# Performance work log

Hardware: AMD Instinct MI355X
Metric: run time of the kernel (lower is better)

Reference implementation:

```python
import jax, jax.numpy as jnp
import numpy as np

N_VERT = 50000
K_NBR = 16          # neighbors per vertex (receptive field = self + K_NBR)
N_MOL = 500
VOCAB = 32
D0 = 64             # initial_hidden


def setup_inputs() -> dict:
    key = jax.random.key(0)
    ks = jax.random.split(key, 10)
    x = jax.random.randint(ks[0], (N_VERT,), 0, VOCAB)
    # receptive field: first entry is the vertex itself (diagonal), then K random neighbors
    nbrs = jax.random.randint(ks[1], (N_VERT, K_NBR), 0, N_VERT)
    rf_vertex = jnp.concatenate([jnp.arange(N_VERT)[:, None], nbrs], axis=1)  # [N, K+1]
    mol_ids = jnp.arange(N_VERT) // (N_VERT // N_MOL)  # sorted molecule segment ids
    embed = jax.random.normal(ks[2], (VOCAB, D0), dtype=jnp.float32)
    W0_0 = jax.random.normal(ks[3], (128, 128), dtype=jnp.float32) * 0.05
    W0_1 = jax.random.normal(ks[4], (128, 64), dtype=jnp.float32) * 0.05
    W1_0 = jax.random.normal(ks[5], (128, 128), dtype=jnp.float32) * 0.05
    W1_1 = jax.random.normal(ks[6], (128, 64), dtype=jnp.float32) * 0.05
    fc_w = jax.random.normal(ks[7], (192, 32), dtype=jnp.float32) * 0.05
    fc_b = jax.random.normal(ks[8], (32,), dtype=jnp.float32) * 0.05
    return {"x": x, "rf_vertex": rf_vertex, "mol_ids": mol_ids, "embed": embed,
            "W0_0": W0_0, "W0_1": W0_1, "W1_0": W1_0, "W1_1": W1_1,
            "fc_w": fc_w, "fc_b": fc_b}


def _ccn_layer(S, rf_vertex, Wa, Wb):
    # S: [N, d] per-vertex summary of previous layer's message.
    # Contraction (nContractions = 2): for RF entry (owner v, vertex w)
    #   c1 = S[w] (gather), c2 = S[v] (owner broadcast)
    N, Kp1 = rf_vertex.shape
    gathered = S[rf_vertex]                               # [N, K+1, d]
    owner = jnp.broadcast_to(S[:, None, :], gathered.shape)
    m = jnp.concatenate([gathered, owner], axis=-1) / Kp1  # normalize by RF size
    h = jax.nn.relu(m @ Wa)                               # per-RF-entry MLP
    h = jax.nn.relu(h @ Wb)                               # [N, K+1, d_out]
    shrunk = h.sum(axis=1)                                # scatter-reduce to vertices
    return h, shrunk


def reference(x, rf_vertex, mol_ids, embed, W0_0, W0_1, W1_0, W1_1, fc_w, fc_b):
    F0 = jax.nn.relu(embed[x])                            # [N, 64]
    _, s0 = _ccn_layer(F0, rf_vertex, W0_0, W0_1)         # [N, 64]
    _, s1 = _ccn_layer(s0, rf_vertex, W1_0, W1_1)         # [N, 64]
    total = jnp.concatenate([F0, s0, s1], axis=1)         # [N, 192]
    rep = jax.ops.segment_sum(total, mol_ids, num_segments=N_MOL)  # [nMol, 192]
    return rep @ fc_w + fc_b                              # [nMol, 32]
```

## Files before the change

### kernel.cpp

```cpp
#include <hip/hip_runtime.h>

#define NV   50000
#define KP1  17
#define NMOL 500
#define VPM  100

typedef __bf16 bf16x8 __attribute__((ext_vector_type(8)));
typedef __bf16 bf16x4 __attribute__((ext_vector_type(4)));
typedef float  f32x4  __attribute__((ext_vector_type(4)));

__device__ __forceinline__ unsigned short f2bf(float f) {
    union { float f; unsigned u; } v; v.f = f;
    return (unsigned short)((v.u + 0x7FFFu + ((v.u >> 16) & 1u)) >> 16);
}

#define MFMA16(a, b, c)  __builtin_amdgcn_mfma_f32_16x16x32_bf16((a), (b), (c), 0, 0, 0)
#define MFMAF8(a, b, c)  __builtin_amdgcn_mfma_f32_16x16x32_fp8_fp8((a), (b), (c), 0, 0, 0)
#define WAITV(n) asm volatile("s_waitcnt vmcnt(" #n ")" ::: "memory")

__device__ __forceinline__ long pk64(unsigned lo, unsigned hi_) {
    return (long)(((unsigned long long)hi_ << 32) | lo);
}

__device__ __forceinline__ void gl_lds16(const void* g, void* l) {
    __builtin_amdgcn_global_load_lds((const __attribute__((address_space(1))) unsigned*)g,
                                     (__attribute__((address_space(3))) unsigned*)l, 16, 0, 0);
}

__device__ __forceinline__ unsigned char f2fp8(float f) {
    int v = __builtin_amdgcn_cvt_pk_fp8_f32(f, 0.f, 0, false);
    return (unsigned char)(v & 0xff);
}

__global__ void prep_weights(const float* __restrict__ W00, const float* __restrict__ W01,
                             const float* __restrict__ W10, const float* __restrict__ W11,
                             unsigned char* __restrict__ WATF0, unsigned char* __restrict__ WATF1,
                             unsigned short* __restrict__ OWT0, unsigned short* __restrict__ OWT1,
                             unsigned short* __restrict__ WbT0, unsigned short* __restrict__ WbT1) {
    int idx = blockIdx.x * 256 + threadIdx.x;
    if (idx >= 8192) return;
    const float sA = 256.0f / 17.0f;
    const float sB = 1.0f / 256.0f;
    {
        int d = idx >> 6, k = idx & 63;
        int tp = (d >> 5) | (((d >> 2) & 1) << 2);
        int rA = ((d >> 3) & 3) * 4 + (d & 3);
        int h = k >> 5, hi = (k >> 3) & 3, j = k & 7;
        int dst = (tp * 64 + hi * 16 + rA) * 16 + h * 8 + j;
        WATF0[dst] = f2fp8(W00[k * 128 + d] * sA);
        WATF1[dst] = f2fp8(W10[k * 128 + d] * sA);
    }
    {
        int d = idx >> 6, k = idx & 63;
        int tp = (d >> 5) | (((d >> 2) & 1) << 2);
        int rA = ((d >> 3) & 3) * 4 + (d & 3);
        int p = tp * 16 + rA;
        OWT0[p * 64 + k] = f2bf(W00[(64 + k) * 128 + d] * sA);
        OWT1[p * 64 + k] = f2bf(W10[(64 + k) * 128 + d] * sA);
    }
    {
        int j = idx >> 7, kk = idx & 127;
        WbT0[idx] = f2bf(W01[kk * 64 + j] * sB);
        WbT1[idx] = f2bf(W11[kk * 64 + j] * sB);
    }
}

template <bool EMBED>
__global__ __launch_bounds__(256) void go_gemm(const int* __restrict__ x,
                                               const float* __restrict__ embed,
                                               const float* __restrict__ S,
                                               const unsigned short* __restrict__ OWT,
                                               float* __restrict__ O,
                                               unsigned char* __restrict__ Sq) {
    int lane = threadIdx.x & 63;
    int wv   = threadIdx.x >> 6;
    int r = lane & 15, hi = lane >> 4;
    int row0 = blockIdx.x * 32 + (wv & 1) * 16;
    int th   = wv >> 1;
    int row  = row0 + r;
    int rowc = row < NV ? row : NV - 1;

    const float* srow = EMBED ? (embed + x[rowc] * 64) : (S + (size_t)rowc * 64);

    float fv[2][8];
    bf16x8 a[2];
#pragma unroll
    for (int c = 0; c < 2; ++c) {
        int k0 = 32 * c + hi * 8;
        float4 f0 = *(const float4*)(srow + k0);
        float4 f1 = *(const float4*)(srow + k0 + 4);
        if (EMBED) {
            f0.x = fmaxf(f0.x, 0.f); f0.y = fmaxf(f0.y, 0.f);
            f0.z = fmaxf(f0.z, 0.f); f0.w = fmaxf(f0.w, 0.f);
            f1.x = fmaxf(f1.x, 0.f); f1.y = fmaxf(f1.y, 0.f);
            f1.z = fmaxf(f1.z, 0.f); f1.w = fmaxf(f1.w, 0.f);
        }
        fv[c][0] = f0.x; fv[c][1] = f0.y; fv[c][2] = f0.z; fv[c][3] = f0.w;
        fv[c][4] = f1.x; fv[c][5] = f1.y; fv[c][6] = f1.z; fv[c][7] = f1.w;
        a[c][0] = (__bf16)f0.x; a[c][1] = (__bf16)f0.y;
        a[c][2] = (__bf16)f0.z; a[c][3] = (__bf16)f0.w;
        a[c][4] = (__bf16)f1.x; a[c][5] = (__bf16)f1.y;
        a[c][6] = (__bf16)f1.z; a[c][7] = (__bf16)f1.w;
    }

    if (th == 0 && row < NV) {
        uint4 q;
        int q0 = __builtin_amdgcn_cvt_pk_fp8_f32(fv[0][0], fv[0][1], 0, false);
        q0     = __builtin_amdgcn_cvt_pk_fp8_f32(fv[0][2], fv[0][3], q0, true);
        int q1 = __builtin_amdgcn_cvt_pk_fp8_f32(fv[0][4], fv[0][5], 0, false);
        q1     = __builtin_amdgcn_cvt_pk_fp8_f32(fv[0][6], fv[0][7], q1, true);
        int q2 = __builtin_amdgcn_cvt_pk_fp8_f32(fv[1][0], fv[1][1], 0, false);
        q2     = __builtin_amdgcn_cvt_pk_fp8_f32(fv[1][2], fv[1][3], q2, true);
        int q3 = __builtin_amdgcn_cvt_pk_fp8_f32(fv[1][4], fv[1][5], 0, false);
        q3     = __builtin_amdgcn_cvt_pk_fp8_f32(fv[1][6], fv[1][7], q3, true);
        q.x = q0; q.y = q1; q.z = q2; q.w = q3;
        *(uint4*)(Sq + (size_t)row * 64 + hi * 16) = q;
    }

#pragma unroll
    for (int ti = 0; ti < 4; ++ti) {
        int t = th * 4 + ti;
        bf16x8 b0 = *(const bf16x8*)(OWT + (16 * t + r) * 64 + hi * 8);
        bf16x8 b1 = *(const bf16x8*)(OWT + (16 * t + r) * 64 + 32 + hi * 8);
        f32x4 acc = {0.f, 0.f, 0.f, 0.f};
        acc = MFMA16(a[0], b0, acc);
        acc = MFMA16(a[1], b1, acc);
#pragma unroll
        for (int q = 0; q < 4; ++q) {
            int orow = row0 + hi * 4 + q;
            if (orow < NV) O[(size_t)orow * 128 + 16 * t + r] = acc[q];
        }
    }
}

__global__ __launch_bounds__(64, 2) void ccn_layer(const unsigned char* __restrict__ Sq,
                                                   const float* __restrict__ O,
                                                   const int* __restrict__ rf,
                                                   const unsigned char* __restrict__ WATF,
                                                   const unsigned short* __restrict__ WbT,
                                                   float* __restrict__ Sout) {
    __shared__ __align__(16) char smem[14336];

    int lane = threadIdx.x;
    int r = lane & 15, hi = lane >> 4;
    int base_v = blockIdx.x * 8;

    char* rfL = smem;
    char* ob  = smem + 1024;
    char* bb  = smem + 5120;
    char* gb  = smem + 6144;

    if (lane < 34) gl_lds16(rf + base_v * KP1 + 4 * lane, rfL);
#pragma unroll
    for (int s = 0; s < 4; ++s) {
        int v = 2 * s + (lane >> 5);
        int ch = lane & 31;
        gl_lds16(O + (size_t)(base_v + v) * 128 + ch * 4, ob + s * 1024);
    }

    long wat[8][2];
#pragma unroll
    for (int tp = 0; tp < 8; ++tp) {
        uint4 w = *(const uint4*)(WATF + (tp * 64 + lane) * 16);
        wat[tp][0] = pk64(w.x, w.y);
        wat[tp][1] = pk64(w.z, w.w);
    }
    bf16x8 bfr[4][4];
#pragma unroll
    for (int c = 0; c < 4; ++c)
#pragma unroll
        for (int t = 0; t < 4; ++t)
            bfr[c][t] = *(const bf16x8*)(WbT + (16 * t + r) * 128 + 32 * c + 8 * hi);

    WAITV(24);

    {
        int rowB = (lane & 31) >> 2;
        int rfB = *(const int*)(rfL + (rowB * KP1 + 16) * 4);
        int clogB = (lane & 3) ^ (rowB & 3);
        gl_lds16(Sq + (size_t)rfB * 64 + clogB * 16, bb);
    }
    {
        int rowA = lane >> 2;
        int clogA = (lane & 3) ^ (rowA & 3);
#pragma unroll 1
        for (int i = 0; i < 8; ++i) {
            int rfv = *(const int*)(rfL + (i * KP1 + rowA) * 4);
            gl_lds16(Sq + (size_t)rfv * 64 + clogA * 16, gb + i * 1024);
        }
    }

#define TILE_CORE(QV, OVLOC, ACC)                                             \
    {                                                                         \
        long bop0 = pk64((QV).x, (QV).y);                                     \
        long bop1 = pk64((QV).z, (QV).w);                                     \
        int ov_ = (OVLOC);                                                    \
        bf16x4 h1v[8];                                                        \
        __builtin_amdgcn_s_setprio(1);                                        \
        _Pragma("unroll")                                                     \
        for (int tp = 0; tp < 8; ++tp) {                                      \
            f32x4 a1 = *(const f32x4*)(ob + ov_ * 512 + tp * 64 + hi * 16);   \
            a1 = MFMAF8(wat[tp][0], bop0, a1);                                \
            a1 = MFMAF8(wat[tp][1], bop1, a1);                                \
            bf16x4 h;                                                         \
            h[0] = (__bf16)fmaxf(a1[0], 0.f);                                 \
            h[1] = (__bf16)fmaxf(a1[1], 0.f);                                 \
            h[2] = (__bf16)fmaxf(a1[2], 0.f);                                 \
            h[3] = (__bf16)fmaxf(a1[3], 0.f);                                 \
            h1v[tp] = h;                                                      \
        }                                                                     \
        _Pragma("unroll")                                                     \
        for (int t = 0; t < 4; ++t) ACC[t] = (f32x4){0.f, 0.f, 0.f, 0.f};     \
        _Pragma("unroll")                                                     \
        for (int c = 0; c < 4; ++c) {                                         \
            bf16x8 afb;                                                       \
            _Pragma("unroll")                                                 \
            for (int j = 0; j < 4; ++j) {                                     \
                afb[j]     = h1v[c][j];                                       \
                afb[4 + j] = h1v[c + 4][j];                                   \
            }                                                                 \
            _Pragma("unroll")                                                 \
            for (int t = 0; t < 4; ++t) ACC[t] = MFMA16(afb, bfr[c][t], ACC[t]); \
        }                                                                     \
        __builtin_amdgcn_s_setprio(0);                                        \
    }

    float bsE[4], bsO[4];
    {
        WAITV(8);
        int srB = r >> 1;
        uint4 qB = *(const uint4*)(bb + srB * 64 + ((hi ^ (srB & 3)) * 16));
        f32x4 aB[4];
        TILE_CORE(qB, srB, aB);
#pragma unroll
        for (int t = 0; t < 4; ++t) {
            bsE[t] = fmaxf(aB[t][0], 0.f);
            bsO[t] = fmaxf(aB[t][2], 0.f);
        }
    }

    float rA0[4] = {0.f, 0.f, 0.f, 0.f};
    float rA1[4] = {0.f, 0.f, 0.f, 0.f};
    WAITV(4);
#pragma unroll 1
    for (int i = 0; i < 4; ++i) {
        uint4 qv = *(const uint4*)(gb + i * 1024 + r * 64 + ((hi ^ (r & 3)) * 16));
        f32x4 acc2[4];
        TILE_CORE(qv, i, acc2);
        bool m0 = (i == hi);
#pragma unroll
        for (int t = 0; t < 4; ++t) {
            float s = fmaxf(acc2[t][0], 0.f) + fmaxf(acc2[t][1], 0.f) +
                      fmaxf(acc2[t][2], 0.f) + fmaxf(acc2[t][3], 0.f);
            s += __shfl_xor(s, 16);
            s += __shfl_xor(s, 32);
            rA0[t] = m0 ? s : rA0[t];
        }
    }
    WAITV(0);
#pragma unroll 1
    for (int i = 4; i < 8; ++i) {
        uint4 qv = *(const uint4*)(gb + i * 1024 + r * 64 + ((hi ^ (r & 3)) * 16));
        f32x4 acc2[4];
        TILE_CORE(qv, i, acc2);
        bool m1 = (i == 4 + hi);
#pragma unroll
        for (int t = 0; t < 4; ++t) {
            float s = fmaxf(acc2[t][0], 0.f) + fmaxf(acc2[t][1], 0.f) +
                      fmaxf(acc2[t][2], 0.f) + fmaxf(acc2[t][3], 0.f);
            s += __shfl_xor(s, 16);
            s += __shfl_xor(s, 32);
            rA1[t] = m1 ? s : rA1[t];
        }
    }

#pragma unroll
    for (int g = 0; g < 2; ++g) {
        int src = r + 16 * (2 * g + (hi >> 1));
#pragma unroll
        for (int t = 0; t < 4; ++t) {
            float asum = g ? rA1[t] : rA0[t];
            float vE = __shfl(bsE[t], src);
            float vO = __shfl(bsO[t], src);
            float bv = (hi & 1) ? vO : vE;
            Sout[(size_t)(base_v + 4 * g + hi) * 64 + 16 * t + r] = asum + bv;
        }
    }
#undef TILE_CORE
}

__global__ void readout(const int* __restrict__ x, const float* __restrict__ embed,
                        const float* __restrict__ s0, const float* __restrict__ s1,
                        const float* __restrict__ fcw, const float* __restrict__ fcb,
                        float* __restrict__ out) {
    __shared__ float rep[192];
    int m = blockIdx.x;
    int c = threadIdx.x;
    int v0 = m * VPM;
    float acc = 0.f;
    if (c < 64) {
#pragma unroll 4
        for (int v = 0; v < VPM; ++v)
            acc += fmaxf(embed[x[v0 + v] * 64 + c], 0.f);
    } else {
        const float* src = (c < 128) ? (s0 + (c - 64)) : (s1 + (c - 128));
#pragma unroll 4
        for (int v = 0; v < VPM; ++v) acc += src[(size_t)(v0 + v) * 64];
    }
    rep[c] = acc;
    __syncthreads();
    if (c < 32) {
        float o = fcb[c];
#pragma unroll 8
        for (int i = 0; i < 192; ++i) o += rep[i] * fcw[i * 32 + c];
        out[m * 32 + c] = o;
    }
}

extern "C" void kernel_launch(void* const* d_in, const int* in_sizes, int n_in,
                              void* d_out, int out_size, void* d_ws, size_t ws_size,
                              hipStream_t stream) {
    const int*   x     = (const int*)d_in[0];
    const int*   rf    = (const int*)d_in[1];
    const float* embed = (const float*)d_in[3];
    const float* W00   = (const float*)d_in[4];
    const float* W01   = (const float*)d_in[5];
    const float* W10   = (const float*)d_in[6];
    const float* W11   = (const float*)d_in[7];
    const float* fcw   = (const float*)d_in[8];
    const float* fcb   = (const float*)d_in[9];
    float* out = (float*)d_out;

    float* s0 = (float*)d_ws;
    float* s1 = s0 + (size_t)NV * 64;
    float* O  = s1 + (size_t)NV * 64;
    unsigned char*  Sq    = (unsigned char*)(O + (size_t)NV * 128);
    unsigned char*  WATF0 = Sq + (size_t)NV * 64;
    unsigned char*  WATF1 = WATF0 + 8192;
    unsigned short* OWT0  = (unsigned short*)(WATF1 + 8192);
    unsigned short* OWT1  = OWT0 + 8192;
    unsigned short* WbT0  = OWT1 + 8192;
    unsigned short* WbT1  = WbT0 + 8192;

    prep_weights<<<32, 256, 0, stream>>>(W00, W01, W10, W11,
                                         WATF0, WATF1, OWT0, OWT1, WbT0, WbT1);

    const int nblk_g = (NV + 31) / 32;
    const int nblk_c = NV / 8;
    go_gemm<true><<<nblk_g, 256, 0, stream>>>(x, embed, nullptr, OWT0, O, Sq);
    ccn_layer<<<nblk_c, 64, 0, stream>>>(Sq, O, rf, WATF0, WbT0, s0);
    go_gemm<false><<<nblk_g, 256, 0, stream>>>(nullptr, nullptr, s0, OWT1, O, Sq);
    ccn_layer<<<nblk_c, 64, 0, stream>>>(Sq, O, rf, WATF1, WbT1, s1);

    readout<<<NMOL, 192, 0, stream>>>(x, embed, s0, s1, fcw, fcb, out);
}
```

Before: 125.4 us.

## Fold owner-half GEMM into fp8 MFMA inside CCN layer, drop O buffer

Removes the separate go_gemm kernel that precomputed the owner contribution S[v]@Wa_owner into a float [N,128] buffer O. The ccn_layer now loads the owner's fp8 row into LDS and does two extra fp8 MFMAs per tile using a widened 128-K weight fragment. Embedding quantisation moves to a per-token lookup table built in prep_weights, and a small sq_quant kernel handles layer two. This cuts roughly 25 MB of O write/read traffic per layer, in exchange for twice the first-stage MFMA work, more weight registers, and fp8 instead of bf16 precision on the owner half.

```diff
diff --git a/kernel.cpp b/kernel.cpp
--- a/kernel.cpp
+++ b/kernel.cpp
@@ -34,136 +34,93 @@
 
 __global__ void prep_weights(const float* __restrict__ W00, const float* __restrict__ W01,
                              const float* __restrict__ W10, const float* __restrict__ W11,
+                             const float* __restrict__ embed,
                              unsigned char* __restrict__ WATF0, unsigned char* __restrict__ WATF1,
-                             unsigned short* __restrict__ OWT0, unsigned short* __restrict__ OWT1,
-                             unsigned short* __restrict__ WbT0, unsigned short* __restrict__ WbT1) {
+                             unsigned short* __restrict__ WbT0, unsigned short* __restrict__ WbT1,
+                             unsigned char* __restrict__ tok_sq) {
     int idx = blockIdx.x * 256 + threadIdx.x;
-    if (idx >= 8192) return;
     const float sA = 256.0f / 17.0f;
     const float sB = 1.0f / 256.0f;
-    {
-        int d = idx >> 6, k = idx & 63;
-        int tp = (d >> 5) | (((d >> 2) & 1) << 2);
-        int rA = ((d >> 3) & 3) * 4 + (d & 3);
-        int h = k >> 5, hi = (k >> 3) & 3, j = k & 7;
-        int dst = (tp * 64 + hi * 16 + rA) * 16 + h * 8 + j;
-        WATF0[dst] = f2fp8(W00[k * 128 + d] * sA);
-        WATF1[dst] = f2fp8(W10[k * 128 + d] * sA);
-    }
-    {
-        int d = idx >> 6, k = idx & 63;
-        int tp = (d >> 5) | (((d >> 2) & 1) << 2);
-        int rA = ((d >> 3) & 3) * 4 + (d & 3);
-        int p = tp * 16 + rA;
-        OWT0[p * 64 + k] = f2bf(W00[(64 + k) * 128 + d] * sA);
-        OWT1[p * 64 + k] = f2bf(W10[(64 + k) * 128 + d] * sA);
-    }
-    {
-        int j = idx >> 7, kk = idx & 127;
-        WbT0[idx] = f2bf(W01[kk * 64 + j] * sB);
-        WbT1[idx] = f2bf(W11[kk * 64 + j] * sB);
-    }
-}
-
-template <bool EMBED>
-__global__ __launch_bounds__(256) void go_gemm(const int* __restrict__ x,
-                                               const float* __restrict__ embed,
-                                               const float* __restrict__ S,
-                                               const unsigned short* __restrict__ OWT,
-                                               float* __restrict__ O,
-                                               unsigned char* __restrict__ Sq) {
-    int lane = threadIdx.x & 63;
-    int wv   = threadIdx.x >> 6;
-    int r = lane & 15, hi = lane >> 4;
-    int row0 = blockIdx.x * 32 + (wv & 1) * 16;
-    int th   = wv >> 1;
-    int row  = row0 + r;
-    int rowc = row < NV ? row : NV - 1;
-
-    const float* srow = EMBED ? (embed + x[rowc] * 64) : (S + (size_t)rowc * 64);
-
-    float fv[2][8];
-    bf16x8 a[2];
-#pragma unroll
-    for (int c = 0; c < 2; ++c) {
-        int k0 = 32 * c + hi * 8;
-        float4 f0 = *(const float4*)(srow + k0);
-        float4 f1 = *(const float4*)(srow + k0 + 4);
-        if (EMBED) {
-            f0.x = fmaxf(f0.x, 0.f); f0.y = fmaxf(f0.y, 0.f);
-            f0.z = fmaxf(f0.z, 0.f); f0.w = fmaxf(f0.w, 0.f);
-            f1.x = fmaxf(f1.x, 0.f); f1.y = fmaxf(f1.y, 0.f);
-            f1.z = fmaxf(f1.z, 0.f); f1.w = fmaxf(f1.w, 0.f);
-        }
-        fv[c][0] = f0.x; fv[c][1] = f0.y; fv[c][2] = f0.z; fv[c][3] = f0.w;
-        fv[c][4] = f1.x; fv[c][5] = f1.y; fv[c][6] = f1.z; fv[c][7] = f1.w;
-        a[c][0] = (__bf16)f0.x; a[c][1] = (__bf16)f0.y;
-        a[c][2] = (__bf16)f0.z; a[c][3] = (__bf16)f0.w;
-        a[c][4] = (__bf16)f1.x; a[c][5] = (__bf16)f1.y;
-        a[c][6] = (__bf16)f1.z; a[c][7] = (__bf16)f1.w;
-    }
-
-    if (th == 0 && row < NV) {
-        uint4 q;
-        int q0 = __builtin_amdgcn_cvt_pk_fp8_f32(fv[0][0], fv[0][1], 0, false);
-        q0     = __builtin_amdgcn_cvt_pk_fp8_f32(fv[0][2], fv[0][3], q0, true);
-        int q1 = __builtin_amdgcn_cvt_pk_fp8_f32(fv[0][4], fv[0][5], 0, false);
-        q1     = __builtin_amdgcn_cvt_pk_fp8_f32(fv[0][6], fv[0][7], q1, true);
-        int q2 = __builtin_amdgcn_cvt_pk_fp8_f32(fv[1][0], fv[1][1], 0, false);
-        q2     = __builtin_amdgcn_cvt_pk_fp8_f32(fv[1][2], fv[1][3], q2, true);
-        int q3 = __builtin_amdgcn_cvt_pk_fp8_f32(fv[1][4], fv[1][5], 0, false);
-        q3     = __builtin_amdgcn_cvt_pk_fp8_f32(fv[1][6], fv[1][7], q3, true);
-        q.x = q0; q.y = q1; q.z = q2; q.w = q3;
-        *(uint4*)(Sq + (size_t)row * 64 + hi * 16) = q;
-    }
-
-#pragma unroll
-    for (int ti = 0; ti < 4; ++ti) {
-        int t = th * 4 + ti;
-        bf16x8 b0 = *(const bf16x8*)(OWT + (16 * t + r) * 64 + hi * 8);
-        bf16x8 b1 = *(const bf16x8*)(OWT + (16 * t + r) * 64 + 32 + hi * 8);
-        f32x4 acc = {0.f, 0.f, 0.f, 0.f};
-        acc = MFMA16(a[0], b0, acc);
-        acc = MFMA16(a[1], b1, acc);
-#pragma unroll
-        for (int q = 0; q < 4; ++q) {
-            int orow = row0 + hi * 4 + q;
-            if (orow < NV) O[(size_t)orow * 128 + 16 * t + r] = acc[q];
-        }
-    }
+    if (idx < 16384) {
+        int j = idx & 7, m = (idx >> 3) & 3, lane = (idx >> 5) & 63, tp = idx >> 11;
+        int rA = lane & 15, hi = lane >> 4;
+        int d = 32 * (tp & 3) + 8 * (rA >> 2) + 4 * (tp >> 2) + (rA & 3);
+        int k = (m >> 1) * 64 + (m & 1) * 32 + 8 * hi + j;
+        WATF0[idx] = f2fp8(W00[k * 128 + d] * sA);
+        WATF1[idx] = f2fp8(W10[k * 128 + d] * sA);
+    }
+    if (idx < 8192) {
+        int jc = idx >> 7, kk = idx & 127;
+        WbT0[idx] = f2bf(W01[kk * 64 + jc] * sB);
+        WbT1[idx] = f2bf(W11[kk * 64 + jc] * sB);
+    }
+    if (idx < 2048) {
+        int tok = idx >> 6, b = idx & 63;
+        int c = b >> 4, bb_ = b & 15;
+        int dim = (bb_ < 8) ? (8 * c + bb_) : (32 + 8 * c + (bb_ - 8));
+        tok_sq[idx] = f2fp8(fmaxf(embed[tok * 64 + dim], 0.f));
+    }
+}
+
+__global__ void sq_embed(const int* __restrict__ x, const unsigned char* __restrict__ tok_sq,
+                         unsigned char* __restrict__ Sq) {
+    int idx = blockIdx.x * 256 + threadIdx.x;
+    if (idx >= NV * 4) return;
+    int n = idx >> 2, c = idx & 3;
+    uint4 v = *(const uint4*)(tok_sq + x[n] * 64 + c * 16);
+    *(uint4*)(Sq + (size_t)n * 64 + c * 16) = v;
+}
+
+__global__ void sq_quant(const float* __restrict__ S, unsigned char* __restrict__ Sq) {
+    int idx = blockIdx.x * 256 + threadIdx.x;
+    if (idx >= NV * 4) return;
+    int n = idx >> 2, c = idx & 3;
+    const float* p = S + (size_t)n * 64;
+    float4 a0 = *(const float4*)(p + 8 * c);
+    float4 a1 = *(const float4*)(p + 8 * c + 4);
+    float4 b0 = *(const float4*)(p + 32 + 8 * c);
+    float4 b1 = *(const float4*)(p + 32 + 8 * c + 4);
+    uint4 q;
+    int t;
+    t = __builtin_amdgcn_cvt_pk_fp8_f32(a0.x, a0.y, 0, false);
+    t = __builtin_amdgcn_cvt_pk_fp8_f32(a0.z, a0.w, t, true);  q.x = t;
+    t = __builtin_amdgcn_cvt_pk_fp8_f32(a1.x, a1.y, 0, false);
+    t = __builtin_amdgcn_cvt_pk_fp8_f32(a1.z, a1.w, t, true);  q.y = t;
+    t = __builtin_amdgcn_cvt_pk_fp8_f32(b0.x, b0.y, 0, false);
+    t = __builtin_amdgcn_cvt_pk_fp8_f32(b0.z, b0.w, t, true);  q.z = t;
+    t = __builtin_amdgcn_cvt_pk_fp8_f32(b1.x, b1.y, 0, false);
+    t = __builtin_amdgcn_cvt_pk_fp8_f32(b1.z, b1.w, t, true);  q.w = t;
+    *(uint4*)(Sq + (size_t)n * 64 + c * 16) = q;
 }
 
 __global__ __launch_bounds__(64, 2) void ccn_layer(const unsigned char* __restrict__ Sq,
-                                                   const float* __restrict__ O,
                                                    const int* __restrict__ rf,
                                                    const unsigned char* __restrict__ WATF,
                                                    const unsigned short* __restrict__ WbT,
                                                    float* __restrict__ Sout) {
-    __shared__ __align__(16) char smem[14336];
+    __shared__ __align__(16) char smem[10752];
 
     int lane = threadIdx.x;
     int r = lane & 15, hi = lane >> 4;
     int base_v = blockIdx.x * 8;
 
-    char* rfL = smem;
-    char* ob  = smem + 1024;
-    char* bb  = smem + 5120;
-    char* gb  = smem + 6144;
+    char* rfL  = smem;
+    char* ownb = smem + 1024;
+    char* bb   = smem + 1536;
+    char* gb   = smem + 2560;
 
     if (lane < 34) gl_lds16(rf + base_v * KP1 + 4 * lane, rfL);
-#pragma unroll
-    for (int s = 0; s < 4; ++s) {
-        int v = 2 * s + (lane >> 5);
-        int ch = lane & 31;
-        gl_lds16(O + (size_t)(base_v + v) * 128 + ch * 4, ob + s * 1024);
-    }
-
-    long wat[8][2];
+    if (lane < 32) gl_lds16(Sq + (size_t)(base_v + (lane >> 2)) * 64 + (lane & 3) * 16, ownb);
+
+    long wat[8][4];
 #pragma unroll
     for (int tp = 0; tp < 8; ++tp) {
-        uint4 w = *(const uint4*)(WATF + (tp * 64 + lane) * 16);
-        wat[tp][0] = pk64(w.x, w.y);
-        wat[tp][1] = pk64(w.z, w.w);
+        uint4 w0 = *(const uint4*)(WATF + (tp * 64 + lane) * 32);
+        uint4 w1 = *(const uint4*)(WATF + (tp * 64 + lane) * 32 + 16);
+        wat[tp][0] = pk64(w0.x, w0.y);
+        wat[tp][1] = pk64(w0.z, w0.w);
+        wat[tp][2] = pk64(w1.x, w1.y);
+        wat[tp][3] = pk64(w1.z, w1.w);
     }
     bf16x8 bfr[4][4];
 #pragma unroll
@@ -172,11 +129,12 @@
         for (int t = 0; t < 4; ++t)
             bfr[c][t] = *(const bf16x8*)(WbT + (16 * t + r) * 128 + 32 * c + 8 * hi);
 
-    WAITV(24);
-
+    WAITV(32);
+
+    const int* rfi = (const int*)rfL;
     {
         int rowB = (lane & 31) >> 2;
-        int rfB = *(const int*)(rfL + (rowB * KP1 + 16) * 4);
+        int rfB = rfi[rowB * KP1 + 16];
         int clogB = (lane & 3) ^ (rowB & 3);
         gl_lds16(Sq + (size_t)rfB * 64 + clogB * 16, bb);
     }
@@ -185,23 +143,27 @@
         int clogA = (lane & 3) ^ (rowA & 3);
 #pragma unroll 1
         for (int i = 0; i < 8; ++i) {
-            int rfv = *(const int*)(rfL + (i * KP1 + rowA) * 4);
+            int rfv = rfi[i * KP1 + rowA];
             gl_lds16(Sq + (size_t)rfv * 64 + clogA * 16, gb + i * 1024);
         }
     }
 
-#define TILE_CORE(QV, OVLOC, ACC)                                             \
+#define TILE_CORE(QV, OWNOFF, ACC)                                            \
     {                                                                         \
         long bop0 = pk64((QV).x, (QV).y);                                     \
         long bop1 = pk64((QV).z, (QV).w);                                     \
-        int ov_ = (OVLOC);                                                    \
+        uint4 ovq = *(const uint4*)(ownb + (OWNOFF));                         \
+        long bop2 = pk64(ovq.x, ovq.y);                                       \
+        long bop3 = pk64(ovq.z, ovq.w);                                       \
         bf16x4 h1v[8];                                                        \
         __builtin_amdgcn_s_setprio(1);                                        \
         _Pragma("unroll")                                                     \
         for (int tp = 0; tp < 8; ++tp) {                                      \
-            f32x4 a1 = *(const f32x4*)(ob + ov_ * 512 + tp * 64 + hi * 16);   \
+            f32x4 a1 = {0.f, 0.f, 0.f, 0.f};                                  \
             a1 = MFMAF8(wat[tp][0], bop0, a1);                                \
             a1 = MFMAF8(wat[tp][1], bop1, a1);                                \
+            a1 = MFMAF8(wat[tp][2], bop2, a1);                                \
+            a1 = MFMAF8(wat[tp][3], bop3, a1);                                \
             bf16x4 h;                                                         \
             h[0] = (__bf16)fmaxf(a1[0], 0.f);                                 \
             h[1] = (__bf16)fmaxf(a1[1], 0.f);                                 \
@@ -231,7 +193,7 @@
         int srB = r >> 1;
         uint4 qB = *(const uint4*)(bb + srB * 64 + ((hi ^ (srB & 3)) * 16));
         f32x4 aB[4];
-        TILE_CORE(qB, srB, aB);
+        TILE_CORE(qB, srB * 64 + hi * 16, aB);
 #pragma unroll
         for (int t = 0; t < 4; ++t) {
             bsE[t] = fmaxf(aB[t][0], 0.f);
@@ -246,7 +208,7 @@
     for (int i = 0; i < 4; ++i) {
         uint4 qv = *(const uint4*)(gb + i * 1024 + r * 64 + ((hi ^ (r & 3)) * 16));
         f32x4 acc2[4];
-        TILE_CORE(qv, i, acc2);
+        TILE_CORE(qv, i * 64 + hi * 16, acc2);
         bool m0 = (i == hi);
 #pragma unroll
         for (int t = 0; t < 4; ++t) {
@@ -262,7 +224,7 @@
     for (int i = 4; i < 8; ++i) {
         uint4 qv = *(const uint4*)(gb + i * 1024 + r * 64 + ((hi ^ (r & 3)) * 16));
         f32x4 acc2[4];
-        TILE_CORE(qv, i, acc2);
+        TILE_CORE(qv, i * 64 + hi * 16, acc2);
         bool m1 = (i == 4 + hi);
 #pragma unroll
         for (int t = 0; t < 4; ++t) {
@@ -333,24 +295,22 @@
 
     float* s0 = (float*)d_ws;
     float* s1 = s0 + (size_t)NV * 64;
-    float* O  = s1 + (size_t)NV * 64;
-    unsigned char*  Sq    = (unsigned char*)(O + (size_t)NV * 128);
+    unsigned char*  Sq    = (unsigned char*)(s1 + (size_t)NV * 64);
     unsigned char*  WATF0 = Sq + (size_t)NV * 64;
-    unsigned char*  WATF1 = WATF0 + 8192;
-    unsigned short* OWT0  = (unsigned short*)(WATF1 + 8192);
-    unsigned short* OWT1  = OWT0 + 8192;
-    unsigned short* WbT0  = OWT1 + 8192;
+    unsigned char*  WATF1 = WATF0 + 16384;
+    unsigned short* WbT0  = (unsigned short*)(WATF1 + 16384);
     unsigned short* WbT1  = WbT0 + 8192;
-
-    prep_weights<<<32, 256, 0, stream>>>(W00, W01, W10, W11,
-                                         WATF0, WATF1, OWT0, OWT1, WbT0, WbT1);
-
-    const int nblk_g = (NV + 31) / 32;
+    unsigned char*  tokq  = (unsigned char*)(WbT1 + 8192);
+
+    prep_weights<<<64, 256, 0, stream>>>(W00, W01, W10, W11, embed,
+                                         WATF0, WATF1, WbT0, WbT1, tokq);
+
+    const int nblk_q = (NV * 4 + 255) / 256;
     const int nblk_c = NV / 8;
-    go_gemm<true><<<nblk_g, 256, 0, stream>>>(x, embed, nullptr, OWT0, O, Sq);
-    ccn_layer<<<nblk_c, 64, 0, stream>>>(Sq, O, rf, WATF0, WbT0, s0);
-    go_gemm<false><<<nblk_g, 256, 0, stream>>>(nullptr, nullptr, s0, OWT1, O, Sq);
-    ccn_layer<<<nblk_c, 64, 0, stream>>>(Sq, O, rf, WATF1, WbT1, s1);
+    sq_embed<<<nblk_q, 256, 0, stream>>>(x, tokq, Sq);
+    ccn_layer<<<nblk_c, 64, 0, stream>>>(Sq, rf, WATF0, WbT0, s0);
+    sq_quant<<<nblk_q, 256, 0, stream>>>(s0, Sq);
+    ccn_layer<<<nblk_c, 64, 0, stream>>>(Sq, rf, WATF1, WbT1, s1);
 
     readout<<<NMOL, 192, 0, stream>>>(x, embed, s0, s1, fcw, fcb, out);
 }
```

After: 117.4 us. -6.4%, faster.
